# Optimization experiments

Hardware: AMD Instinct MI355X
Metric: run time of the kernel (lower is better)

The kernel has to match this reference:

```python
import jax, jax.numpy as jnp
import numpy as np

KH = KW = 3
STRIDE = 1
ITERATIONS = 2
EPS = 1e-7


def _squash(s):
    # squash along last axis (capsule dim)
    sn = jnp.sum(s * s, axis=-1, keepdims=True)
    return (sn / (1.0 + sn)) * s / jnp.sqrt(sn + EPS)


def setup_inputs() -> dict:
    key = jax.random.key(0)
    k1, k2 = jax.random.split(key)
    x = jax.random.normal(k1, (4, 14, 14, 32, 8), dtype=jnp.float32)
    # W: [1,1,1,filters_out, caps_per_patch=3*3*32, dims_out=16, dims_in=8], stddev=0.1 init
    W = 0.1 * jax.random.normal(k2, (1, 1, 1, 32, 288, 16, 8), dtype=jnp.float32)
    return {"x": x, "W": W}


def reference(x, W):
    B, H, Wd, Fin, Din = x.shape
    Ho = (H - KH) // STRIDE + 1
    Wo = (Wd - KW) // STRIDE + 1
    # Patch extraction, channel order (kh, kw, Fin) to match tf.image.extract_patches
    patches = jnp.stack(
        [x[:, i:i + Ho * STRIDE:STRIDE, j:j + Wo * STRIDE:STRIDE]
         for i in range(KH) for j in range(KW)],
        axis=3,
    )  # [B,Ho,Wo,KH*KW,Fin,Din]
    patches = patches.reshape(B, Ho, Wo, KH * KW * Fin, Din)  # [B,Ho,Wo,C,Di]

    Wm = W[0, 0, 0]  # [F, C, Do, Di]
    F, C, Do, _ = Wm.shape
    # predictions[b,h,w,f,c,o] = sum_i W[f,c,o,i] * patches[b,h,w,c,i]
    preds = jnp.einsum('fcoi,bhwci->bhwfco', Wm, patches)

    logits = jnp.zeros((B, Ho, Wo, F, C), dtype=preds.dtype)
    outputs = jnp.zeros((B, Ho, Wo, F, Do), dtype=preds.dtype)
    for _ in range(ITERATIONS):
        # agreement = predictions^T @ outputs over the dims_out axis
        agreement = jnp.einsum('bhwfco,bhwfo->bhwfc', preds, outputs)
        logits = logits + agreement
        # NOTE: original code softmaxes over axis=3 (the filters_out axis)
        cc = jax.nn.softmax(logits, axis=3)  # [B,Ho,Wo,F,C]
        centroids = jnp.sum(cc[..., None] * preds, axis=4)  # [B,Ho,Wo,F,Do]
        outputs = _squash(centroids)
    return outputs
```

## Files before the change

### kernel.cpp

```cpp
#include <hip/hip_runtime.h>

#define NB   4
#define H_IN 14
#define W_IN 14
#define FIN  32
#define DI   8
#define F    32
#define C    288
#define DO   16
#define HO   12
#define WO   12
#define NPOS (NB*HO*WO)
#define EPS  1e-7f

#define CH   16
#define CC   (C/CH)

#define XELE  (NB*H_IN*W_IN*FIN*DI)
#define W2H_BYTES  ((size_t)F*C*DO*DI*2)
#define XH_BYTES   ((size_t)XELE*2)
#define CENT_BYTES ((size_t)NPOS*F*DO*4)
#define PART_BYTES ((size_t)CH*CENT_BYTES)
#define OUT1_BYTES CENT_BYTES

typedef _Float16 h2 __attribute__((ext_vector_type(2)));

__device__ __forceinline__ unsigned int pack2(float a, float b) {
    h2 v; v.x = (_Float16)a; v.y = (_Float16)b;
    return __builtin_bit_cast(unsigned int, v);
}

__device__ __forceinline__ float dot8h(const uint4 w, const uint4 v, float acc) {
#if __has_builtin(__builtin_amdgcn_fdot2)
    acc = __builtin_amdgcn_fdot2(__builtin_bit_cast(h2, w.x), __builtin_bit_cast(h2, v.x), acc, false);
    acc = __builtin_amdgcn_fdot2(__builtin_bit_cast(h2, w.y), __builtin_bit_cast(h2, v.y), acc, false);
    acc = __builtin_amdgcn_fdot2(__builtin_bit_cast(h2, w.z), __builtin_bit_cast(h2, v.z), acc, false);
    acc = __builtin_amdgcn_fdot2(__builtin_bit_cast(h2, w.w), __builtin_bit_cast(h2, v.w), acc, false);
#else
    const h2 w0 = __builtin_bit_cast(h2, w.x), v0 = __builtin_bit_cast(h2, v.x);
    const h2 w1 = __builtin_bit_cast(h2, w.y), v1 = __builtin_bit_cast(h2, v.y);
    const h2 w2 = __builtin_bit_cast(h2, w.z), v2 = __builtin_bit_cast(h2, v.z);
    const h2 w3 = __builtin_bit_cast(h2, w.w), v3 = __builtin_bit_cast(h2, v.w);
    acc += (float)w0.x*(float)v0.x + (float)w0.y*(float)v0.y
         + (float)w1.x*(float)v1.x + (float)w1.y*(float)v1.y
         + (float)w2.x*(float)v2.x + (float)w2.y*(float)v2.y
         + (float)w3.x*(float)v3.x + (float)w3.y*(float)v3.y;
#endif
    return acc;
}

__device__ __forceinline__ int xbase_of(int pos) {
    const int b = pos/(HO*WO), rem = pos%(HO*WO), ho = rem/WO, wo = rem%WO;
    return ((b*H_IN + ho)*W_IN + wo)*FIN*DI;
}

__device__ __forceinline__ void stage_xh(const unsigned short* __restrict__ xh,
                                         uint4 (*xs4)[8],
                                         const int ch, const int pg, const int tid) {
    if (tid < CC*8) {
        const int cl = tid >> 3, p = tid & 7;
        const int c  = ch*CC + cl;
        const int slab = c >> 5, fin = c & 31;
        const int kh = slab/3, kw = slab%3;
        const int off = xbase_of(pg*8 + p) + (kh*W_IN + kw)*FIN*DI + fin*DI;
        xs4[cl][p] = *(const uint4*)(xh + off);
    }
}

__global__ __launch_bounds__(256) void kernTh(const float* __restrict__ Wt,
                                              unsigned short* __restrict__ W2h) {
    const int idx = blockIdx.x*256 + threadIdx.x;
    const int f = idx & 31, o = (idx >> 5) & 15, c = idx >> 9;
    const float* src = Wt + ((size_t)(f*C + c)*DO + o)*DI;
    const float4 a = *(const float4*)src;
    const float4 b = *(const float4*)(src + 4);
    uint4 r;
    r.x = pack2(a.x, a.y); r.y = pack2(a.z, a.w);
    r.z = pack2(b.x, b.y); r.w = pack2(b.z, b.w);
    ((uint4*)W2h)[idx] = r;
}

__global__ __launch_bounds__(256) void kernXh(const float* __restrict__ x,
                                              unsigned short* __restrict__ xh) {
    const int i = blockIdx.x*256 + threadIdx.x;
    const float4 v = ((const float4*)x)[i];
    uint2 o;
    o.x = pack2(v.x, v.y); o.y = pack2(v.z, v.w);
    ((uint2*)xh)[i] = o;
}

__global__ __launch_bounds__(256, 4) void kern1n(const unsigned short* __restrict__ xh,
                                                 const unsigned short* __restrict__ W2h,
                                                 float* __restrict__ part1)
{
    __shared__ uint4 xs4[CC][8];
    const int tid = threadIdx.x;
    const int f  = tid & 31;
    const int og = tid >> 5;
    const int o0 = 2*og, o1 = o0 + 1;
    const int ch = blockIdx.x & (CH-1);
    const int pg = blockIdx.x >> 4;

    stage_xh(xh, xs4, ch, pg, tid);
    __syncthreads();

    const uint4* W2h4 = (const uint4*)W2h;
    const int c0 = ch*CC;

    float acc0[8], acc1[8];
    #pragma unroll
    for (int p = 0; p < 8; ++p) { acc0[p] = 0.f; acc1[p] = 0.f; }

    #pragma unroll 1
    for (int cl = 0; cl < CC; ++cl) {
        const int c = c0 + cl;
        const uint4 w0 = W2h4[(size_t)(c*DO + o0)*F + f];
        const uint4 w1 = W2h4[(size_t)(c*DO + o1)*F + f];
        #pragma unroll
        for (int p = 0; p < 8; ++p) {
            const uint4 xv = xs4[cl][p];
            acc0[p] = dot8h(w0, xv, acc0[p]);
            acc1[p] = dot8h(w1, xv, acc1[p]);
        }
    }
    #pragma unroll
    for (int p = 0; p < 8; ++p) {
        const size_t base = ((size_t)(ch*NPOS + pg*8 + p))*DO;
        part1[(base + o0)*F + f] = acc0[p];
        part1[(base + o1)*F + f] = acc1[p];
    }
}

__global__ __launch_bounds__(512) void kernO(const float* __restrict__ part1,
                                             float* __restrict__ out1)
{
    __shared__ float red[512];
    const int pos = blockIdx.x, tid = threadIdx.x;
    const int f = tid & 31, o = tid >> 5;

    float s = 0.f;
    #pragma unroll
    for (int k = 0; k < CH; ++k)
        s += part1[(size_t)(k*NPOS + pos)*512 + tid];
    s *= (1.f/32.f);

    red[tid] = s*s;
    __syncthreads();
    if (tid < 256) red[tid] += red[tid + 256];
    __syncthreads();
    if (tid < 128) red[tid] += red[tid + 128];
    __syncthreads();
    if (tid < 64)  red[tid] += red[tid + 64];
    __syncthreads();
    if (tid < 32) {
        const float sn = red[tid] + red[tid + 32];
        red[tid] = (sn/(1.f + sn)) * rsqrtf(sn + EPS);
    }
    __syncthreads();
    out1[(size_t)pos*512 + f*DO + o] = s * red[f];
}

__global__ __launch_bounds__(256) void kern2n(const unsigned short* __restrict__ xh,
                                              const unsigned short* __restrict__ W2h,
                                              const float* __restrict__ out1,
                                              float* __restrict__ part2)
{
    __shared__ uint4 xs4[CC][8];
    __shared__ float red[2][4][8][32];
    __shared__ float ccs[2][8][32];

    const int tid = threadIdx.x;
    const int f  = tid & 31;
    const int og = tid >> 5;
    const int o0 = 2*og, o1 = o0 + 1;
    const int wv = tid >> 6;
    const int half = (tid >> 5) & 1;
    const int ch = blockIdx.x & (CH-1);
    const int pg = blockIdx.x >> 4;

    stage_xh(xh, xs4, ch, pg, tid);

    float u0[8], u1[8];
    #pragma unroll
    for (int p = 0; p < 8; ++p) {
        const float* up = out1 + (size_t)(pg*8 + p)*512 + f*DO;
        u0[p] = up[o0];
        u1[p] = up[o1];
    }

    const uint4* W2h4 = (const uint4*)W2h;
    const int c0 = ch*CC;

    float acc0[8], acc1[8];
    #pragma unroll
    for (int p = 0; p < 8; ++p) { acc0[p] = 0.f; acc1[p] = 0.f; }

    __syncthreads();

    #pragma unroll 1
    for (int cl = 0; cl < CC; ++cl) {
        const int c = c0 + cl;
        const int buf = cl & 1;
        const uint4 w0 = W2h4[(size_t)(c*DO + o0)*F + f];
        const uint4 w1 = W2h4[(size_t)(c*DO + o1)*F + f];

        float pred0[8], pred1[8];
        #pragma unroll
        for (int p = 0; p < 8; ++p) {
            const uint4 xv = xs4[cl][p];
            pred0[p] = dot8h(w0, xv, 0.f);
            pred1[p] = dot8h(w1, xv, 0.f);
        }

        #pragma unroll
        for (int p = 0; p < 8; ++p) {
            float ap = pred0[p]*u0[p] + pred1[p]*u1[p];
            ap += __shfl_xor(ap, 32);
            if (half == 0) red[buf][wv][p][f] = ap;
        }
        __syncthreads();

        {
            const int p2 = tid >> 5, f2 = tid & 31;
            const float agr = red[buf][0][p2][f2] + red[buf][1][p2][f2]
                            + red[buf][2][p2][f2] + red[buf][3][p2][f2];
            float m = agr;
            m = fmaxf(m, __shfl_xor(m, 1));
            m = fmaxf(m, __shfl_xor(m, 2));
            m = fmaxf(m, __shfl_xor(m, 4));
            m = fmaxf(m, __shfl_xor(m, 8));
            m = fmaxf(m, __shfl_xor(m, 16));
            const float e = __expf(agr - m);
            float s = e;
            s += __shfl_xor(s, 1);
            s += __shfl_xor(s, 2);
            s += __shfl_xor(s, 4);
            s += __shfl_xor(s, 8);
            s += __shfl_xor(s, 16);
            ccs[buf][p2][f2] = e / s;
        }
        __syncthreads();

        #pragma unroll
        for (int p = 0; p < 8; ++p) {
            const float cv = ccs[buf][p][f];
            acc0[p] += cv*pred0[p];
            acc1[p] += cv*pred1[p];
        }
    }

    #pragma unroll
    for (int p = 0; p < 8; ++p) {
        const size_t base = ((size_t)(ch*NPOS + pg*8 + p))*DO;
        part2[(base + o0)*F + f] = acc0[p];
        part2[(base + o1)*F + f] = acc1[p];
    }
}

__global__ __launch_bounds__(256) void kern3(const float* __restrict__ part2,
                                             float* __restrict__ out)
{
    const int tid = threadIdx.x;
    const int f = tid & 31, p = tid >> 5;
    const int pos = blockIdx.x*8 + p;

    float cent[DO];
    #pragma unroll
    for (int o = 0; o < DO; ++o) cent[o] = 0.f;
    #pragma unroll 1
    for (int k = 0; k < CH; ++k) {
        const float* s = part2 + (size_t)(k*NPOS + pos)*512 + f;
        #pragma unroll
        for (int o = 0; o < DO; ++o) cent[o] += s[o*F];
    }
    float sn = 0.f;
    #pragma unroll
    for (int o = 0; o < DO; ++o) sn += cent[o]*cent[o];
    const float sc = (sn/(1.f + sn)) * rsqrtf(sn + EPS);
    float* dst = out + ((size_t)pos*F + f)*DO;
    #pragma unroll
    for (int o = 0; o < DO; ++o) dst[o] = cent[o]*sc;
}

__device__ __forceinline__ float dot8(const float4* __restrict__ w,
                                      const float4 p0, const float4 p1) {
    float4 a = w[0], b = w[1];
    return a.x*p0.x + a.y*p0.y + a.z*p0.z + a.w*p0.w
         + b.x*p1.x + b.y*p1.y + b.z*p1.z + b.w*p1.w;
}

__global__ __launch_bounds__(256) void capsule_kernel_f32(
    const float* __restrict__ x, const float* __restrict__ Wt,
    float* __restrict__ out)
{
    __shared__ float patch[C*DI];
    __shared__ float cent[F*DO];
    __shared__ float out1[F*DO];
    __shared__ float agr[F*C];
    __shared__ float scale_s[F];

    const int tid = threadIdx.x;
    const int pos = blockIdx.x;
    const int b   = pos / (HO*WO);
    const int rem = pos % (HO*WO);
    const int ho  = rem / WO;
    const int wo  = rem % WO;

    #pragma unroll
    for (int slab = 0; slab < 9; ++slab) {
        const int kh = slab / 3, kw = slab % 3;
        const float* src = x + (((b*H_IN + ho + kh)*W_IN + (wo + kw))*FIN)*DI;
        patch[slab*256 + tid] = src[tid];
    }
    __syncthreads();

    const float4* pv = (const float4*)patch;

    {
        const int fo0 = tid, fo1 = tid + 256;
        const int f0 = fo0 >> 4, o0 = fo0 & 15;
        const int f1 = fo1 >> 4, o1 = fo1 & 15;
        float acc0 = 0.f, acc1 = 0.f;
        for (int c = 0; c < C; ++c) {
            const float4 p0 = pv[c*2], p1 = pv[c*2+1];
            acc0 += dot8((const float4*)(Wt + ((f0*C + c)*DO + o0)*DI), p0, p1);
            acc1 += dot8((const float4*)(Wt + ((f1*C + c)*DO + o1)*DI), p0, p1);
        }
        cent[fo0] = acc0 * (1.f/32.f);
        cent[fo1] = acc1 * (1.f/32.f);
    }
    __syncthreads();

    if (tid < F) {
        float sn = 0.f;
        #pragma unroll
        for (int o = 0; o < DO; ++o) { float v = cent[tid*DO + o]; sn += v*v; }
        const float sc = (sn/(1.f + sn)) * rsqrtf(sn + EPS);
        #pragma unroll
        for (int o = 0; o < DO; ++o) out1[tid*DO + o] = cent[tid*DO + o] * sc;
    }
    __syncthreads();

    #pragma unroll 1
    for (int r = 0; r < (F*C)/256; ++r) {
        const int pp = tid + 256*r;
        const int f = pp / C, c = pp % C;
        const float4* wrow = (const float4*)(Wt + (f*C + c)*DO*DI);
        const float4 p0 = pv[c*2], p1 = pv[c*2+1];
        float a = 0.f;
        #pragma unroll
        for (int o = 0; o < DO; ++o) a += dot8(wrow + o*2, p0, p1) * out1[f*DO + o];
        agr[pp] = a;
    }
    __syncthreads();

    for (int c = tid; c < C; c += 256) {
        float m = -1e30f;
        #pragma unroll
        for (int f = 0; f < F; ++f) m = fmaxf(m, agr[f*C + c]);
        float s = 0.f;
        #pragma unroll
        for (int f = 0; f < F; ++f) {
            const float e = __expf(agr[f*C + c] - m);
            agr[f*C + c] = e; s += e;
        }
        const float inv = 1.f / s;
        #pragma unroll
        for (int f = 0; f < F; ++f) agr[f*C + c] *= inv;
    }
    __syncthreads();

    {
        const int fo0 = tid, fo1 = tid + 256;
        const int f0 = fo0 >> 4, o0 = fo0 & 15;
        const int f1 = fo1 >> 4, o1 = fo1 & 15;
        float acc0 = 0.f, acc1 = 0.f;
        for (int c = 0; c < C; ++c) {
            const float4 p0 = pv[c*2], p1 = pv[c*2+1];
            acc0 += agr[f0*C + c] * dot8((const float4*)(Wt + ((f0*C + c)*DO + o0)*DI), p0, p1);
            acc1 += agr[f1*C + c] * dot8((const float4*)(Wt + ((f1*C + c)*DO + o1)*DI), p0, p1);
        }
        cent[fo0] = acc0;
        cent[fo1] = acc1;
    }
    __syncthreads();

    if (tid < F) {
        float sn = 0.f;
        #pragma unroll
        for (int o = 0; o < DO; ++o) { float v = cent[tid*DO + o]; sn += v*v; }
        scale_s[tid] = (sn/(1.f + sn)) * rsqrtf(sn + EPS);
    }
    __syncthreads();

    out[pos*(F*DO) + tid]       = cent[tid]       * scale_s[tid >> 4];
    out[pos*(F*DO) + tid + 256] = cent[tid + 256] * scale_s[(tid >> 4) + 16];
}

extern "C" void kernel_launch(void* const* d_in, const int* in_sizes, int n_in,
                              void* d_out, int out_size, void* d_ws, size_t ws_size,
                              hipStream_t stream) {
    const float* x  = (const float*)d_in[0];
    const float* Wt = (const float*)d_in[1];
    float* out = (float*)d_out;

    if (ws_size >= W2H_BYTES + XH_BYTES + PART_BYTES + OUT1_BYTES) {
        unsigned short* W2h = (unsigned short*)d_ws;
        unsigned short* xh  = (unsigned short*)((char*)d_ws + W2H_BYTES);
        float* part1 = (float*)((char*)d_ws + W2H_BYTES + XH_BYTES);
        float* out1  = (float*)((char*)d_ws + W2H_BYTES + XH_BYTES + PART_BYTES);
        kernTh<<<(F*C*DO)/256*1, 256, 0, stream>>>(Wt, W2h);
        kernXh<<<XELE/4/256, 256, 0, stream>>>(x, xh);
        kern1n<<<CH*(NPOS/8), 256, 0, stream>>>(xh, W2h, part1);
        kernO<<<NPOS, 512, 0, stream>>>(part1, out1);
        kern2n<<<CH*(NPOS/8), 256, 0, stream>>>(xh, W2h, out1, part1);
        kern3<<<NPOS/8, 256, 0, stream>>>(part1, out);
    } else {
        capsule_kernel_f32<<<NPOS, 256, 0, stream>>>(x, Wt, out);
    }
}
```

Baseline: 146.0 us.

## Remap kern2n threads to position-per-warp, removing block syncs; fuse conversion kernels

kern2n now gives each warp one position and each lane one filter, with all 16 output dims held in registers. The agreement and softmax over filters are computed entirely with warp shuffles, which removes the two per-capsule __syncthreads and the shared-memory reduction. The partial-output layout becomes [ch,pos,f,o] so that kern2n and kern3 can use float4 stores and loads, and the two fp32-to-half conversion kernels are merged into one launch. In exchange, each thread now loads 16 W vectors per capsule instead of 2, which raises register pressure and the amount of W fetched per thread.

Result: slower. 150.7 us (+3.2%).

```diff
diff --git a/kernel.cpp b/kernel.cpp
--- a/kernel.cpp
+++ b/kernel.cpp
@@ -67,26 +67,30 @@
     }
 }
 
-__global__ __launch_bounds__(256) void kernTh(const float* __restrict__ Wt,
-                                              unsigned short* __restrict__ W2h) {
-    const int idx = blockIdx.x*256 + threadIdx.x;
-    const int f = idx & 31, o = (idx >> 5) & 15, c = idx >> 9;
-    const float* src = Wt + ((size_t)(f*C + c)*DO + o)*DI;
-    const float4 a = *(const float4*)src;
-    const float4 b = *(const float4*)(src + 4);
-    uint4 r;
-    r.x = pack2(a.x, a.y); r.y = pack2(a.z, a.w);
-    r.z = pack2(b.x, b.y); r.w = pack2(b.z, b.w);
-    ((uint4*)W2h)[idx] = r;
-}
-
-__global__ __launch_bounds__(256) void kernXh(const float* __restrict__ x,
-                                              unsigned short* __restrict__ xh) {
-    const int i = blockIdx.x*256 + threadIdx.x;
-    const float4 v = ((const float4*)x)[i];
-    uint2 o;
-    o.x = pack2(v.x, v.y); o.y = pack2(v.z, v.w);
-    ((uint2*)xh)[i] = o;
+__global__ __launch_bounds__(256) void kernConv(const float* __restrict__ Wt,
+                                                unsigned short* __restrict__ W2h,
+                                                const float* __restrict__ x,
+                                                unsigned short* __restrict__ xh) {
+    const int b = blockIdx.x;
+    if (b < (F*C*DO)/256) {
+        const int idx = b*256 + threadIdx.x;
+        const int f = idx & 31, o = (idx >> 5) & 15, c = idx >> 9;
+        const float* src = Wt + ((size_t)(f*C + c)*DO + o)*DI;
+        const float4 a = *(const float4*)src;
+        const float4 bb = *(const float4*)(src + 4);
+        uint4 r;
+        r.x = pack2(a.x, a.y);  r.y = pack2(a.z, a.w);
+        r.z = pack2(bb.x, bb.y); r.w = pack2(bb.z, bb.w);
+        ((uint4*)W2h)[idx] = r;
+    } else {
+        const int i = (b - (F*C*DO)/256)*256 + threadIdx.x;
+        if (i < XELE/4) {
+            const float4 v = ((const float4*)x)[i];
+            uint2 o;
+            o.x = pack2(v.x, v.y); o.y = pack2(v.z, v.w);
+            ((uint2*)xh)[i] = o;
+        }
+    }
 }
 
 __global__ __launch_bounds__(256, 4) void kern1n(const unsigned short* __restrict__ xh,
@@ -166,95 +170,83 @@
                                               float* __restrict__ part2)
 {
     __shared__ uint4 xs4[CC][8];
-    __shared__ float red[2][4][8][32];
-    __shared__ float ccs[2][8][32];
-
     const int tid = threadIdx.x;
     const int f  = tid & 31;
-    const int og = tid >> 5;
-    const int o0 = 2*og, o1 = o0 + 1;
-    const int wv = tid >> 6;
-    const int half = (tid >> 5) & 1;
+    const int pp = tid >> 5;
     const int ch = blockIdx.x & (CH-1);
     const int pg = blockIdx.x >> 4;
+    const int pos = pg*8 + pp;
 
     stage_xh(xh, xs4, ch, pg, tid);
 
-    float u0[8], u1[8];
-    #pragma unroll
-    for (int p = 0; p < 8; ++p) {
-        const float* up = out1 + (size_t)(pg*8 + p)*512 + f*DO;
-        u0[p] = up[o0];
-        u1[p] = up[o1];
-    }
+    float o1[DO];
+    {
+        const float4* s = (const float4*)(out1 + (size_t)pos*512 + f*DO);
+        #pragma unroll
+        for (int q = 0; q < 4; ++q) {
+            const float4 v = s[q];
+            o1[4*q+0] = v.x; o1[4*q+1] = v.y; o1[4*q+2] = v.z; o1[4*q+3] = v.w;
+        }
+    }
+    __syncthreads();
 
     const uint4* W2h4 = (const uint4*)W2h;
     const int c0 = ch*CC;
 
-    float acc0[8], acc1[8];
-    #pragma unroll
-    for (int p = 0; p < 8; ++p) { acc0[p] = 0.f; acc1[p] = 0.f; }
-
-    __syncthreads();
+    float acc[DO];
+    #pragma unroll
+    for (int o = 0; o < DO; ++o) acc[o] = 0.f;
 
     #pragma unroll 1
     for (int cl = 0; cl < CC; ++cl) {
         const int c = c0 + cl;
-        const int buf = cl & 1;
-        const uint4 w0 = W2h4[(size_t)(c*DO + o0)*F + f];
-        const uint4 w1 = W2h4[(size_t)(c*DO + o1)*F + f];
-
-        float pred0[8], pred1[8];
-        #pragma unroll
-        for (int p = 0; p < 8; ++p) {
-            const uint4 xv = xs4[cl][p];
-            pred0[p] = dot8h(w0, xv, 0.f);
-            pred1[p] = dot8h(w1, xv, 0.f);
-        }
-
-        #pragma unroll
-        for (int p = 0; p < 8; ++p) {
-            float ap = pred0[p]*u0[p] + pred1[p]*u1[p];
-            ap += __shfl_xor(ap, 32);
-            if (half == 0) red[buf][wv][p][f] = ap;
-        }
-        __syncthreads();
-
+        const uint4 xv = xs4[cl][pp];
+        const uint4* wb = W2h4 + (size_t)c*DO*F + f;
+
+        float pred[DO];
         {
-            const int p2 = tid >> 5, f2 = tid & 31;
-            const float agr = red[buf][0][p2][f2] + red[buf][1][p2][f2]
-                            + red[buf][2][p2][f2] + red[buf][3][p2][f2];
-            float m = agr;
-            m = fmaxf(m, __shfl_xor(m, 1));
-            m = fmaxf(m, __shfl_xor(m, 2));
-            m = fmaxf(m, __shfl_xor(m, 4));
-            m = fmaxf(m, __shfl_xor(m, 8));
-            m = fmaxf(m, __shfl_xor(m, 16));
-            const float e = __expf(agr - m);
-            float s = e;
-            s += __shfl_xor(s, 1);
-            s += __shfl_xor(s, 2);
-            s += __shfl_xor(s, 4);
-            s += __shfl_xor(s, 8);
-            s += __shfl_xor(s, 16);
-            ccs[buf][p2][f2] = e / s;
-        }
-        __syncthreads();
-
-        #pragma unroll
-        for (int p = 0; p < 8; ++p) {
-            const float cv = ccs[buf][p][f];
-            acc0[p] += cv*pred0[p];
-            acc1[p] += cv*pred1[p];
-        }
-    }
-
-    #pragma unroll
-    for (int p = 0; p < 8; ++p) {
-        const size_t base = ((size_t)(ch*NPOS + pg*8 + p))*DO;
-        part2[(base + o0)*F + f] = acc0[p];
-        part2[(base + o1)*F + f] = acc1[p];
-    }
+            uint4 w[8];
+            #pragma unroll
+            for (int o = 0; o < 8; ++o) w[o] = wb[o*F];
+            #pragma unroll
+            for (int o = 0; o < 8; ++o) pred[o] = dot8h(w[o], xv, 0.f);
+        }
+        {
+            uint4 w[8];
+            #pragma unroll
+            for (int o = 0; o < 8; ++o) w[o] = wb[(o+8)*F];
+            #pragma unroll
+            for (int o = 0; o < 8; ++o) pred[8+o] = dot8h(w[o], xv, 0.f);
+        }
+
+        float agr = 0.f;
+        #pragma unroll
+        for (int o = 0; o < DO; ++o) agr += pred[o]*o1[o];
+
+        float m = agr;
+        m = fmaxf(m, __shfl_xor(m, 1));
+        m = fmaxf(m, __shfl_xor(m, 2));
+        m = fmaxf(m, __shfl_xor(m, 4));
+        m = fmaxf(m, __shfl_xor(m, 8));
+        m = fmaxf(m, __shfl_xor(m, 16));
+        const float e = __expf(agr - m);
+        float s = e;
+        s += __shfl_xor(s, 1);
+        s += __shfl_xor(s, 2);
+        s += __shfl_xor(s, 4);
+        s += __shfl_xor(s, 8);
+        s += __shfl_xor(s, 16);
+        const float cc = e / s;
+
+        #pragma unroll
+        for (int o = 0; o < DO; ++o) acc[o] += cc*pred[o];
+    }
+
+    float4* d = (float4*)(part2 + ((size_t)(ch*NPOS + pos)*F + f)*DO);
+    d[0] = make_float4(acc[0],  acc[1],  acc[2],  acc[3]);
+    d[1] = make_float4(acc[4],  acc[5],  acc[6],  acc[7]);
+    d[2] = make_float4(acc[8],  acc[9],  acc[10], acc[11]);
+    d[3] = make_float4(acc[12], acc[13], acc[14], acc[15]);
 }
 
 __global__ __launch_bounds__(256) void kern3(const float* __restrict__ part2,
@@ -267,19 +259,25 @@
     float cent[DO];
     #pragma unroll
     for (int o = 0; o < DO; ++o) cent[o] = 0.f;
-    #pragma unroll 1
+    #pragma unroll
     for (int k = 0; k < CH; ++k) {
-        const float* s = part2 + (size_t)(k*NPOS + pos)*512 + f;
-        #pragma unroll
-        for (int o = 0; o < DO; ++o) cent[o] += s[o*F];
+        const float4* s = (const float4*)(part2 + ((size_t)(k*NPOS + pos)*F + f)*DO);
+        #pragma unroll
+        for (int q = 0; q < 4; ++q) {
+            const float4 v = s[q];
+            cent[q*4+0] += v.x; cent[q*4+1] += v.y;
+            cent[q*4+2] += v.z; cent[q*4+3] += v.w;
+        }
     }
     float sn = 0.f;
     #pragma unroll
     for (int o = 0; o < DO; ++o) sn += cent[o]*cent[o];
     const float sc = (sn/(1.f + sn)) * rsqrtf(sn + EPS);
-    float* dst = out + ((size_t)pos*F + f)*DO;
-    #pragma unroll
-    for (int o = 0; o < DO; ++o) dst[o] = cent[o]*sc;
+    float4* dst = (float4*)(out + ((size_t)pos*F + f)*DO);
+    dst[0] = make_float4(cent[0]*sc,  cent[1]*sc,  cent[2]*sc,  cent[3]*sc);
+    dst[1] = make_float4(cent[4]*sc,  cent[5]*sc,  cent[6]*sc,  cent[7]*sc);
+    dst[2] = make_float4(cent[8]*sc,  cent[9]*sc,  cent[10]*sc, cent[11]*sc);
+    dst[3] = make_float4(cent[12]*sc, cent[13]*sc, cent[14]*sc, cent[15]*sc);
 }
 
 __device__ __forceinline__ float dot8(const float4* __restrict__ w,
@@ -409,8 +407,7 @@
         unsigned short* xh  = (unsigned short*)((char*)d_ws + W2H_BYTES);
         float* part1 = (float*)((char*)d_ws + W2H_BYTES + XH_BYTES);
         float* out1  = (float*)((char*)d_ws + W2H_BYTES + XH_BYTES + PART_BYTES);
-        kernTh<<<(F*C*DO)/256*1, 256, 0, stream>>>(Wt, W2h);
-        kernXh<<<XELE/4/256, 256, 0, stream>>>(x, xh);
+        kernConv<<<(F*C*DO)/256 + XELE/4/256, 256, 0, stream>>>(Wt, W2h, x, xh);
         kern1n<<<CH*(NPOS/8), 256, 0, stream>>>(xh, W2h, part1);
         kernO<<<NPOS, 512, 0, stream>>>(part1, out1);
         kern2n<<<CH*(NPOS/8), 256, 0, stream>>>(xh, W2h, out1, part1);
```

## Merge conversion kernels and read patches directly from global instead of LDS staging

Applied to the files above, without the earlier changes.

Fuses the weight and input fp16 conversion kernels into one launch, removing one kernel launch. In both prediction kernels, drops the shared-memory staging of input patches and the barrier that follows it; each thread now loads its patch vectors straight from global memory through per-position offsets. The shared copy was wide-broadcast and cheap, so the new uniform global loads depend on cache hits, and each thread issues more memory requests per channel than before.

Result: faster. 142.7 us (-2.2%).

```diff
diff --git a/kernel.cpp b/kernel.cpp
--- a/kernel.cpp
+++ b/kernel.cpp
@@ -54,46 +54,42 @@
     return ((b*H_IN + ho)*W_IN + wo)*FIN*DI;
 }
 
-__device__ __forceinline__ void stage_xh(const unsigned short* __restrict__ xh,
-                                         uint4 (*xs4)[8],
-                                         const int ch, const int pg, const int tid) {
-    if (tid < CC*8) {
-        const int cl = tid >> 3, p = tid & 7;
-        const int c  = ch*CC + cl;
-        const int slab = c >> 5, fin = c & 31;
-        const int kh = slab/3, kw = slab%3;
-        const int off = xbase_of(pg*8 + p) + (kh*W_IN + kw)*FIN*DI + fin*DI;
-        xs4[cl][p] = *(const uint4*)(xh + off);
-    }
-}
-
-__global__ __launch_bounds__(256) void kernTh(const float* __restrict__ Wt,
-                                              unsigned short* __restrict__ W2h) {
-    const int idx = blockIdx.x*256 + threadIdx.x;
-    const int f = idx & 31, o = (idx >> 5) & 15, c = idx >> 9;
-    const float* src = Wt + ((size_t)(f*C + c)*DO + o)*DI;
-    const float4 a = *(const float4*)src;
-    const float4 b = *(const float4*)(src + 4);
-    uint4 r;
-    r.x = pack2(a.x, a.y); r.y = pack2(a.z, a.w);
-    r.z = pack2(b.x, b.y); r.w = pack2(b.z, b.w);
-    ((uint4*)W2h)[idx] = r;
-}
-
-__global__ __launch_bounds__(256) void kernXh(const float* __restrict__ x,
-                                              unsigned short* __restrict__ xh) {
-    const int i = blockIdx.x*256 + threadIdx.x;
-    const float4 v = ((const float4*)x)[i];
-    uint2 o;
-    o.x = pack2(v.x, v.y); o.y = pack2(v.z, v.w);
-    ((uint2*)xh)[i] = o;
+__device__ __forceinline__ int coff_of(int c) {
+    const int slab = c >> 5, fin = c & 31;
+    const int kh = slab/3, kw = slab%3;
+    return (kh*W_IN + kw)*FIN*DI + fin*DI;
+}
+
+__global__ __launch_bounds__(256) void kernConv(const float* __restrict__ Wt,
+                                                unsigned short* __restrict__ W2h,
+                                                const float* __restrict__ x,
+                                                unsigned short* __restrict__ xh) {
+    const int b = blockIdx.x;
+    if (b < (F*C*DO)/256) {
+        const int idx = b*256 + threadIdx.x;
+        const int f = idx & 31, o = (idx >> 5) & 15, c = idx >> 9;
+        const float* src = Wt + ((size_t)(f*C + c)*DO + o)*DI;
+        const float4 a = *(const float4*)src;
+        const float4 bb = *(const float4*)(src + 4);
+        uint4 r;
+        r.x = pack2(a.x, a.y);  r.y = pack2(a.z, a.w);
+        r.z = pack2(bb.x, bb.y); r.w = pack2(bb.z, bb.w);
+        ((uint4*)W2h)[idx] = r;
+    } else {
+        const int i = (b - (F*C*DO)/256)*256 + threadIdx.x;
+        if (i < XELE/4) {
+            const float4 v = ((const float4*)x)[i];
+            uint2 o;
+            o.x = pack2(v.x, v.y); o.y = pack2(v.z, v.w);
+            ((uint2*)xh)[i] = o;
+        }
+    }
 }
 
 __global__ __launch_bounds__(256, 4) void kern1n(const unsigned short* __restrict__ xh,
                                                  const unsigned short* __restrict__ W2h,
                                                  float* __restrict__ part1)
 {
-    __shared__ uint4 xs4[CC][8];
     const int tid = threadIdx.x;
     const int f  = tid & 31;
     const int og = tid >> 5;
@@ -101,8 +97,9 @@
     const int ch = blockIdx.x & (CH-1);
     const int pg = blockIdx.x >> 4;
 
-    stage_xh(xh, xs4, ch, pg, tid);
-    __syncthreads();
+    int xoff[8];
+    #pragma unroll
+    for (int p = 0; p < 8; ++p) xoff[p] = xbase_of(pg*8 + p);
 
     const uint4* W2h4 = (const uint4*)W2h;
     const int c0 = ch*CC;
@@ -114,11 +111,12 @@
     #pragma unroll 1
     for (int cl = 0; cl < CC; ++cl) {
         const int c = c0 + cl;
+        const int coff = coff_of(c);
         const uint4 w0 = W2h4[(size_t)(c*DO + o0)*F + f];
         const uint4 w1 = W2h4[(size_t)(c*DO + o1)*F + f];
         #pragma unroll
         for (int p = 0; p < 8; ++p) {
-            const uint4 xv = xs4[cl][p];
+            const uint4 xv = *(const uint4*)(xh + xoff[p] + coff);
             acc0[p] = dot8h(w0, xv, acc0[p]);
             acc1[p] = dot8h(w1, xv, acc1[p]);
         }
@@ -165,7 +163,6 @@
                                               const float* __restrict__ out1,
                                               float* __restrict__ part2)
 {
-    __shared__ uint4 xs4[CC][8];
     __shared__ float red[2][4][8][32];
     __shared__ float ccs[2][8][32];
 
@@ -178,7 +175,9 @@
     const int ch = blockIdx.x & (CH-1);
     const int pg = blockIdx.x >> 4;
 
-    stage_xh(xh, xs4, ch, pg, tid);
+    int xoff[8];
+    #pragma unroll
+    for (int p = 0; p < 8; ++p) xoff[p] = xbase_of(pg*8 + p);
 
     float u0[8], u1[8];
     #pragma unroll
@@ -195,19 +194,18 @@
     #pragma unroll
     for (int p = 0; p < 8; ++p) { acc0[p] = 0.f; acc1[p] = 0.f; }
 
-    __syncthreads();
-
     #pragma unroll 1
     for (int cl = 0; cl < CC; ++cl) {
         const int c = c0 + cl;
         const int buf = cl & 1;
+        const int coff = coff_of(c);
         const uint4 w0 = W2h4[(size_t)(c*DO + o0)*F + f];
         const uint4 w1 = W2h4[(size_t)(c*DO + o1)*F + f];
 
         float pred0[8], pred1[8];
         #pragma unroll
         for (int p = 0; p < 8; ++p) {
-            const uint4 xv = xs4[cl][p];
+            const uint4 xv = *(const uint4*)(xh + xoff[p] + coff);
             pred0[p] = dot8h(w0, xv, 0.f);
             pred1[p] = dot8h(w1, xv, 0.f);
         }
@@ -409,8 +407,7 @@
         unsigned short* xh  = (unsigned short*)((char*)d_ws + W2H_BYTES);
         float* part1 = (float*)((char*)d_ws + W2H_BYTES + XH_BYTES);
         float* out1  = (float*)((char*)d_ws + W2H_BYTES + XH_BYTES + PART_BYTES);
-        kernTh<<<(F*C*DO)/256*1, 256, 0, stream>>>(Wt, W2h);
-        kernXh<<<XELE/4/256, 256, 0, stream>>>(x, xh);
+        kernConv<<<(F*C*DO)/256 + XELE/4/256, 256, 0, stream>>>(Wt, W2h, x, xh);
         kern1n<<<CH*(NPOS/8), 256, 0, stream>>>(xh, W2h, part1);
         kernO<<<NPOS, 512, 0, stream>>>(part1, out1);
         kern2n<<<CH*(NPOS/8), 256, 0, stream>>>(xh, W2h, out1, part1);
```
